# Performance work log

Hardware: AMD Instinct MI355X
Metric: run time of the kernel (lower is better)

Reference implementation:

```python
import jax, jax.numpy as jnp
import numpy as np
import math

B = 1048576
BG_RES = 512
NUM_LEVELS = 2
POWER = 4
MIPNOISE = 0.5
INIT_VAL = -2.0


def cube_face_uv(v):
    # v: [N,3] direction vectors. OpenGL cubemap face convention
    # (faces: 0:+x 1:-x 2:+y 3:-y 4:+z 5:-z), as used by nvdiffrast 'cube'.
    x, y, z = v[:, 0], v[:, 1], v[:, 2]
    ax, ay, az = jnp.abs(x), jnp.abs(y), jnp.abs(z)
    is_x = (ax >= ay) & (ax >= az)
    is_y = (~is_x) & (ay >= az)
    face = jnp.where(is_x, jnp.where(x >= 0, 0, 1),
                     jnp.where(is_y, jnp.where(y >= 0, 2, 3),
                               jnp.where(z >= 0, 4, 5))).astype(jnp.int32)
    ma = jnp.where(is_x, ax, jnp.where(is_y, ay, az))
    sc = jnp.where(is_x, jnp.where(x >= 0, -z, z),
                   jnp.where(is_y, x, jnp.where(z >= 0, x, -x)))
    tc = jnp.where(is_x, -y, jnp.where(is_y, jnp.where(y >= 0, z, -z), -y))
    u = 0.5 * (sc / ma + 1.0)
    t = 0.5 * (tc / ma + 1.0)
    return face, u, t


def build_pyramid(tex):
    # tex: [6,R,R,3] -> list of 2x2 box-filtered mips down to 1x1 (nvdiffrast style)
    levels = [tex]
    t = tex
    while t.shape[1] > 1:
        R = t.shape[1]
        t = t.reshape(6, R // 2, 2, R // 2, 2, 3).mean(axis=(2, 4))
        levels.append(t)
    return levels


def bilinear(tex, face, u, v):
    # tex: [6,R,R,3]; face/u/v: [N]. Clamp-to-edge bilinear per selected face.
    R = tex.shape[1]
    x = u * R - 0.5
    y = v * R - 0.5
    x0f = jnp.floor(x); y0f = jnp.floor(y)
    fx = (x - x0f)[:, None]; fy = (y - y0f)[:, None]
    x0 = jnp.clip(x0f.astype(jnp.int32), 0, R - 1)
    y0 = jnp.clip(y0f.astype(jnp.int32), 0, R - 1)
    x1 = jnp.clip(x0f.astype(jnp.int32) + 1, 0, R - 1)
    y1 = jnp.clip(y0f.astype(jnp.int32) + 1, 0, R - 1)
    flat = tex.reshape(6 * R * R, 3)
    base = face * (R * R)
    g00 = flat[base + y0 * R + x0]
    g01 = flat[base + y0 * R + x1]
    g10 = flat[base + y1 * R + x0]
    g11 = flat[base + y1 * R + x1]
    return ((1 - fx) * (1 - fy) * g00 + fx * (1 - fy) * g01 +
            (1 - fx) * fy * g10 + fx * fy * g11)


def sample_cubemap(tex6, face, u, v, mip):
    # trilinear: bilinear in two adjacent mips, lerp by fractional mip level
    levels = build_pyramid(tex6)
    lmax = float(len(levels) - 1)
    m = jnp.clip(mip, 0.0, lmax)
    out = jnp.zeros((face.shape[0], 3), tex6.dtype)
    for l, t in enumerate(levels):
        wl = jnp.clip(1.0 - jnp.abs(m - l), 0.0, 1.0)  # (1-f)/f trilinear weights
        out = out + wl[:, None] * bilinear(t, face, u, v)
    return out


def setup_inputs() -> dict:
    key = jax.random.key(0)
    k1, k2, k3, k4, k5 = jax.random.split(key, 5)
    viewdirs = jax.random.normal(k1, (B, 3), dtype=jnp.float32)
    viewdirs = viewdirs / jnp.linalg.norm(viewdirs, axis=-1, keepdims=True)
    saSample = jax.random.normal(k2, (B,), dtype=jnp.float32)
    noise_u = jax.random.uniform(k3, (B,), dtype=jnp.float32)
    # parameters (init_val*ones/(num_levels-i) in torch; perturbed for nontrivial grads)
    bg_mat0 = (INIT_VAL * jnp.ones((1, 6, 128, 128, 3), jnp.float32)
               + 0.1 * jax.random.normal(k4, (1, 6, 128, 128, 3), jnp.float32))
    bg_mat1 = (INIT_VAL / 2.0 * jnp.ones((1, 6, 512, 512, 3), jnp.float32)
               + 0.1 * jax.random.normal(k5, (1, 6, 512, 512, 3), jnp.float32))
    return {
        "viewdirs": viewdirs,
        "saSample": saSample,
        "noise_u": noise_u,
        "bg_mat0": bg_mat0,
        "bg_mat1": bg_mat1,
        "brightness": jnp.asarray(0.0, jnp.float32),
        "mul": jnp.asarray(1.0, jnp.float32),
        "mipbias": jnp.asarray(0.5, jnp.float32),
    }


def reference(viewdirs, saSample, noise_u, bg_mat0, bg_mat1, brightness, mul, mipbias):
    h = w = BG_RES  # from bg_mats[-1]
    # sa2mip
    distortion = 1.0 / jnp.max(jnp.abs(viewdirs), axis=-1)  # 1/||u||_inf
    saTexel = distortion / h / w
    miplevel = ((saSample - jnp.log(saTexel)) / math.log(POWER) / 2.0
                + mipbias + MIPNOISE * noise_u)
    miplevel = jnp.maximum(miplevel, 0.0)

    face, u, t = cube_face_uv(viewdirs)
    sumemb = sample_cubemap(bg_mat0[0], face, u, t, miplevel)  # mip 1 (128)
    sumemb = sumemb + sample_cubemap(bg_mat1[0], face, u, t, miplevel)  # mip 0 (512)

    # activation == 'identity' branch: exp(x).clip(0.01, 1000)
    img = jnp.clip(jnp.exp(jnp.clip(brightness, -1.0, 2.0) + mul * sumemb), 0.01, 1000.0)
    return img
```

## Files before the change

### kernel.cpp

```cpp
#include <hip/hip_runtime.h>
#include <hip/hip_bf16.h>
#include <math.h>


#define NPYR1_4 524286

__device__ __constant__ int OFFS0[7] = {0, 24576, 30720, 32256, 32640, 32736, 32760};
__device__ __constant__ int OFFS1[9] = {0, 393216, 491520, 516096, 522240,
                                        523776, 524160, 524256, 524280};
static const int H_OFFS0[7] = {0, 24576, 30720, 32256, 32640, 32736, 32760};
static const int H_OFFS1[9] = {0, 393216, 491520, 516096, 522240,
                               523776, 524160, 524256, 524280};

__device__ __constant__ int LOFF[5] = {0, 1536, 1920, 2016, 2040};

struct PyrArgs {
    const void* src;
    float4* dst[5];
    int R;
    int tpf;
    int T;
    int nlev;
};

__global__ __launch_bounds__(256) void pyr_kernel(PyrArgs a0, PyrArgs a1, int split) {
    __shared__ float4 A[32 * 32];
    __shared__ float4 Bb[16 * 16];

    PyrArgs a = (blockIdx.x < (unsigned)split) ? a0 : a1;
    int bid = (blockIdx.x < (unsigned)split) ? blockIdx.x : blockIdx.x - split;

    const int tpf = a.tpf;
    const int face = bid / (tpf * tpf);
    const int tif = bid - face * tpf * tpf;
    const int ty = tif / tpf, tx = tif - (tif / tpf) * tpf;
    const int T = a.T, R = a.R;
    const int tid = threadIdx.x;
    const int baseY = ty * T, baseX = tx * T;

    const int total = T * T;
    const float* src = (const float*)a.src;
    for (int idx = tid; idx < total; idx += 256) {
        int r = idx / T, c = idx - (idx / T) * T;
        const float* p = src + ((size_t)(face * R + baseY + r) * R + baseX + c) * 3;
        A[r * T + c] = make_float4(p[0], p[1], p[2], 0.f);
    }
    __syncthreads();

    float4* cur = A;
    float4* nxt = Bb;
    int curT = T;
    for (int l = 0; l < a.nlev; ++l) {
        const int nT = curT >> 1;
        const int Rg = R >> (l + 1);
        const int tb = T >> (l + 1);
        float4* dst = a.dst[l];
        const int n = nT * nT;
        for (int idx = tid; idx < n; idx += 256) {
            int ly = idx / nT, lx = idx - (idx / nT) * nT;
            float4 q00 = cur[(2 * ly) * curT + 2 * lx];
            float4 q01 = cur[(2 * ly) * curT + 2 * lx + 1];
            float4 q10 = cur[(2 * ly + 1) * curT + 2 * lx];
            float4 q11 = cur[(2 * ly + 1) * curT + 2 * lx + 1];
            float4 s = make_float4(0.25f * (q00.x + q01.x + q10.x + q11.x),
                                   0.25f * (q00.y + q01.y + q10.y + q11.y),
                                   0.25f * (q00.z + q01.z + q10.z + q11.z), 0.f);
            nxt[ly * nT + lx] = s;
            dst[(size_t)(face * Rg + ty * tb + ly) * Rg + tx * tb + lx] = s;
        }
        __syncthreads();
        float4* tmp = cur; cur = nxt; nxt = tmp;
        curT = nT;
    }
}


__device__ __forceinline__ void wuv(int R, float u, float v, int& x0, int& x1,
                                    int& y0, int& y1, float& fx, float& fy) {
    float xf = u * (float)R - 0.5f;
    float yf = v * (float)R - 0.5f;
    float x0f = floorf(xf), y0f = floorf(yf);
    fx = xf - x0f;
    fy = yf - y0f;
    int xi = (int)x0f, yi = (int)y0f;
    x0 = min(max(xi, 0), R - 1);
    x1 = min(max(xi + 1, 0), R - 1);
    y0 = min(max(yi, 0), R - 1);
    y1 = min(max(yi + 1, 0), R - 1);
}

__device__ __forceinline__ void bilin4(const float4* __restrict__ tex, int R,
                                       int face, float u, float v, float o[3]) {
    int x0, x1, y0, y1; float fx, fy;
    wuv(R, u, v, x0, x1, y0, y1, fx, fy);
    const float4* base = tex + (size_t)face * R * R;
    float4 p00 = base[y0 * R + x0];
    float4 p01 = base[y0 * R + x1];
    float4 p10 = base[y1 * R + x0];
    float4 p11 = base[y1 * R + x1];
    float w00 = (1.f - fx) * (1.f - fy), w01 = fx * (1.f - fy);
    float w10 = (1.f - fx) * fy, w11 = fx * fy;
    o[0] = w00 * p00.x + w01 * p01.x + w10 * p10.x + w11 * p11.x;
    o[1] = w00 * p00.y + w01 * p01.y + w10 * p10.y + w11 * p11.y;
    o[2] = w00 * p00.z + w01 * p01.z + w10 * p10.z + w11 * p11.z;
}

__device__ __forceinline__ void bilin3(const float* __restrict__ tex, int R,
                                       int face, float u, float v, float o[3]) {
    int x0, x1, y0, y1; float fx, fy;
    wuv(R, u, v, x0, x1, y0, y1, fx, fy);
    const float* base = tex + (size_t)face * R * R * 3;
    const float* p00 = base + (y0 * R + x0) * 3;
    const float* p01 = base + (y0 * R + x1) * 3;
    const float* p10 = base + (y1 * R + x0) * 3;
    const float* p11 = base + (y1 * R + x1) * 3;
    float w00 = (1.f - fx) * (1.f - fy), w01 = fx * (1.f - fy);
    float w10 = (1.f - fx) * fy, w11 = fx * fy;
#pragma unroll
    for (int c = 0; c < 3; ++c)
        o[c] = w00 * p00[c] + w01 * p01[c] + w10 * p10[c] + w11 * p11[c];
}

__device__ __forceinline__ void bilinL(const float4* __restrict__ L, int lb, int R,
                                       int face, float u, float v, float o[3]) {
    int x0, x1, y0, y1; float fx, fy;
    wuv(R, u, v, x0, x1, y0, y1, fx, fy);
    const float4* base = L + lb + face * R * R;
    float4 p00 = base[y0 * R + x0];
    float4 p01 = base[y0 * R + x1];
    float4 p10 = base[y1 * R + x0];
    float4 p11 = base[y1 * R + x1];
    float w00 = (1.f - fx) * (1.f - fy), w01 = fx * (1.f - fy);
    float w10 = (1.f - fx) * fy, w11 = fx * fy;
    o[0] = w00 * p00.x + w01 * p01.x + w10 * p10.x + w11 * p11.x;
    o[1] = w00 * p00.y + w01 * p01.y + w10 * p10.y + w11 * p11.y;
    o[2] = w00 * p00.z + w01 * p01.z + w10 * p10.z + w11 * p11.z;
}

__device__ __forceinline__ void tap1(const float4* __restrict__ L,
                                     const float* __restrict__ tex1,
                                     const float4* __restrict__ pyr1, int l,
                                     int face, float u, float v, float o[3]) {
    if (l >= 5)      bilinL(L, LOFF[l - 5], 16 >> (l - 5), face, u, v, o);
    else if (l >= 1) bilin4(pyr1 + OFFS1[l - 1], 512 >> l, face, u, v, o);
    else             bilin3(tex1, 512, face, u, v, o);
}

__device__ __forceinline__ void tap0(const float4* __restrict__ L,
                                     const float* __restrict__ tex0,
                                     const float4* __restrict__ pyr0, int l,
                                     int face, float u, float v, float o[3]) {
    if (l >= 3)      bilinL(L, 2046 + LOFF[l - 3], 16 >> (l - 3), face, u, v, o);
    else if (l >= 1) bilin4(pyr0 + OFFS0[l - 1], 128 >> l, face, u, v, o);
    else             bilin3(tex0, 128, face, u, v, o);
}

__device__ __forceinline__ void lds_reduce(float4* L, int sb, int sr, int db,
                                           int tid) {
    int dr = sr >> 1;
    int n = 6 * dr * dr;
    for (int idx = tid; idx < n; idx += 256) {
        int f = idx / (dr * dr);
        int rem = idx - f * dr * dr;
        int y = rem / dr, x = rem - y * dr;
        const float4* s = L + sb + f * sr * sr;
        float4 q00 = s[(2 * y) * sr + 2 * x];
        float4 q01 = s[(2 * y) * sr + 2 * x + 1];
        float4 q10 = s[(2 * y + 1) * sr + 2 * x];
        float4 q11 = s[(2 * y + 1) * sr + 2 * x + 1];
        L[db + f * dr * dr + y * dr + x] =
            make_float4(0.25f * (q00.x + q01.x + q10.x + q11.x),
                        0.25f * (q00.y + q01.y + q10.y + q11.y),
                        0.25f * (q00.z + q01.z + q10.z + q11.z), 0.f);
    }
}

__global__ __launch_bounds__(256) void sample_kernel(
    const float* __restrict__ vd, const float* __restrict__ sa,
    const float* __restrict__ nu, const float* __restrict__ tex0,
    const float* __restrict__ tex1, const float* __restrict__ sb,
    const float* __restrict__ sm, const float* __restrict__ smb,
    const float4* __restrict__ pyr0, const float4* __restrict__ pyr1,
    float* __restrict__ out, int n) {
    __shared__ float4 L[4092];
    const int tid = threadIdx.x;

    for (int i = tid; i < 1536; i += 256) L[i] = pyr1[OFFS1[4] + i];
    for (int i = tid; i < 1536; i += 256) L[2046 + i] = pyr0[OFFS0[2] + i];
    for (int i = tid; i < 384; i += 256)  L[3582 + i] = pyr0[OFFS0[3] + i];
    for (int i = tid; i < 96; i += 256)   L[3966 + i] = pyr0[OFFS0[4] + i];
    __syncthreads();
    lds_reduce(L, 0, 16, 1536, tid);
    lds_reduce(L, 3966, 4, 4062, tid);
    __syncthreads();
    lds_reduce(L, 1536, 8, 1920, tid);
    lds_reduce(L, 4062, 2, 4086, tid);
    __syncthreads();
    lds_reduce(L, 1920, 4, 2016, tid);
    __syncthreads();
    lds_reduce(L, 2016, 2, 2040, tid);
    __syncthreads();

    const float brightness = fminf(fmaxf(sb[0], -1.f), 2.f);
    const float mul = sm[0];
    const float mipbias = smb[0];

    const int stride = gridDim.x * 256;
    for (int i = blockIdx.x * 256 + tid; i < n; i += stride) {
        float x = vd[3 * i + 0];
        float y = vd[3 * i + 1];
        float z = vd[3 * i + 2];
        float ax = fabsf(x), ay = fabsf(y), az = fabsf(z);

        bool is_x = (ax >= ay) && (ax >= az);
        bool is_y = (!is_x) && (ay >= az);

        int face;
        float ma, sc, tc;
        if (is_x) {
            face = (x >= 0.f) ? 0 : 1;
            ma = ax; sc = (x >= 0.f) ? -z : z; tc = -y;
        } else if (is_y) {
            face = (y >= 0.f) ? 2 : 3;
            ma = ay; sc = x; tc = (y >= 0.f) ? z : -z;
        } else {
            face = (z >= 0.f) ? 4 : 5;
            ma = az; sc = (z >= 0.f) ? x : -x; tc = -y;
        }
        float u = 0.5f * (sc / ma + 1.f);
        float t = 0.5f * (tc / ma + 1.f);

        float saTexel = (1.f / ma) / 512.f / 512.f;
        float mip = (sa[i] - logf(saTexel)) / 1.3862943611198906f / 2.0f +
                    mipbias + 0.5f * nu[i];
        mip = fmaxf(mip, 0.f);

        float s0[3];
        {
            float m = fminf(mip, 7.f);
            float l0f = floorf(m);
            int l0 = (int)l0f;
            float f = m - l0f;
            tap0(L, tex0, pyr0, l0, face, u, t, s0);
            if (f > 0.f && l0 < 7) {
                float c1[3];
                tap0(L, tex0, pyr0, l0 + 1, face, u, t, c1);
                float w0 = 1.f - f;
#pragma unroll
                for (int c = 0; c < 3; ++c) s0[c] = w0 * s0[c] + f * c1[c];
            }
        }
        float s1[3];
        {
            float m = fminf(mip, 9.f);
            float l0f = floorf(m);
            int l0 = (int)l0f;
            float f = m - l0f;
            tap1(L, tex1, pyr1, l0, face, u, t, s1);
            if (f > 0.f && l0 < 9) {
                float c1[3];
                tap1(L, tex1, pyr1, l0 + 1, face, u, t, c1);
                float w0 = 1.f - f;
#pragma unroll
                for (int c = 0; c < 3; ++c) s1[c] = w0 * s1[c] + f * c1[c];
            }
        }

#pragma unroll
        for (int c = 0; c < 3; ++c) {
            float e = expf(brightness + mul * (s0[c] + s1[c]));
            out[3 * i + c] = fminf(fmaxf(e, 0.01f), 1000.f);
        }
    }
}

extern "C" void kernel_launch(void* const* d_in, const int* in_sizes, int n_in,
                              void* d_out, int out_size, void* d_ws, size_t ws_size,
                              hipStream_t stream) {
    const float* vd = (const float*)d_in[0];
    const float* sa = (const float*)d_in[1];
    const float* nu = (const float*)d_in[2];
    const float* tex0 = (const float*)d_in[3];
    const float* tex1 = (const float*)d_in[4];
    const float* br = (const float*)d_in[5];
    const float* mu = (const float*)d_in[6];
    const float* mb = (const float*)d_in[7];
    float* out = (float*)d_out;

    float4* pyr1 = (float4*)d_ws;
    float4* pyr0 = pyr1 + NPYR1_4;

    const int B = in_sizes[1];

    PyrArgs a0{}, a1{};
    a0.src = tex1; a0.R = 512; a0.tpf = 16; a0.T = 32; a0.nlev = 5;
    for (int l = 0; l < 5; ++l) a0.dst[l] = pyr1 + H_OFFS1[l];
    a1.src = tex0; a1.R = 128; a1.tpf = 4; a1.T = 32; a1.nlev = 5;
    for (int l = 0; l < 5; ++l) a1.dst[l] = pyr0 + H_OFFS0[l];
    int split1 = 6 * 16 * 16;
    int grid1 = split1 + 6 * 4 * 4;
    hipLaunchKernelGGL(pyr_kernel, dim3(grid1), dim3(256), 0, stream, a0, a1, split1);

    hipLaunchKernelGGL(sample_kernel, dim3(512), dim3(256), 0, stream,
                       vd, sa, nu, tex0, tex1, br, mu, mb, pyr0, pyr1, out, B);
}
```

Measured before the change: 143.3 us.

## Store mip pyramid in fp16, vectorize texture staging, enlarge sample grid

Mip pyramid levels in workspace and the LDS-resident small levels are now stored as packed 4x fp16 (8 bytes) instead of float4, halving gather bandwidth and LDS footprint. Pyramid tile loading reads base texels with float4 vector loads. Level offsets become closed-form expressions instead of constant-memory tables, and the sample kernel grid grows from 512 to 1280 blocks. The cost is fp16 rounding of filtered texels, including compounded rounding in the LDS reductions, which may affect accuracy.

```diff
diff --git a/kernel.cpp b/kernel.cpp
--- a/kernel.cpp
+++ b/kernel.cpp
@@ -1,22 +1,23 @@
 #include <hip/hip_runtime.h>
 #include <hip/hip_bf16.h>
+#include <hip/hip_fp16.h>
 #include <math.h>
 
 
-#define NPYR1_4 524286
-
-__device__ __constant__ int OFFS0[7] = {0, 24576, 30720, 32256, 32640, 32736, 32760};
-__device__ __constant__ int OFFS1[9] = {0, 393216, 491520, 516096, 522240,
-                                        523776, 524160, 524256, 524280};
-static const int H_OFFS0[7] = {0, 24576, 30720, 32256, 32640, 32736, 32760};
-static const int H_OFFS1[9] = {0, 393216, 491520, 516096, 522240,
-                               523776, 524160, 524256, 524280};
-
-__device__ __constant__ int LOFF[5] = {0, 1536, 1920, 2016, 2040};
+struct __align__(8) H4 { __half x, y, z, w; };
+
+#define PYR0_WS_BASE 524288
+
+__device__ __forceinline__ H4 f2h4(float a, float b, float c) {
+    H4 h;
+    h.x = __float2half(a); h.y = __float2half(b); h.z = __float2half(c);
+    h.w = __float2half(0.f);
+    return h;
+}
 
 struct PyrArgs {
-    const void* src;
-    float4* dst[5];
+    const float* src;
+    H4* dst[5];
     int R;
     int tpf;
     int T;
@@ -38,12 +39,17 @@
     const int tid = threadIdx.x;
     const int baseY = ty * T, baseX = tx * T;
 
-    const int total = T * T;
-    const float* src = (const float*)a.src;
-    for (int idx = tid; idx < total; idx += 256) {
-        int r = idx / T, c = idx - (idx / T) * T;
-        const float* p = src + ((size_t)(face * R + baseY + r) * R + baseX + c) * 3;
-        A[r * T + c] = make_float4(p[0], p[1], p[2], 0.f);
+    const int ngroups = (T * T) >> 2;
+    for (int g = tid; g < ngroups; g += 256) {
+        int r = (g * 4) / T, c = (g * 4) - ((g * 4) / T) * T;
+        const float4* p = (const float4*)(a.src +
+            ((size_t)(face * R + baseY + r) * R + baseX + c) * 3);
+        float4 q0 = p[0], q1 = p[1], q2 = p[2];
+        float4* dst = &A[r * T + c];
+        dst[0] = make_float4(q0.x, q0.y, q0.z, 0.f);
+        dst[1] = make_float4(q0.w, q1.x, q1.y, 0.f);
+        dst[2] = make_float4(q1.z, q1.w, q2.x, 0.f);
+        dst[3] = make_float4(q2.y, q2.z, q2.w, 0.f);
     }
     __syncthreads();
 
@@ -54,7 +60,7 @@
         const int nT = curT >> 1;
         const int Rg = R >> (l + 1);
         const int tb = T >> (l + 1);
-        float4* dst = a.dst[l];
+        H4* dst = a.dst[l];
         const int n = nT * nT;
         for (int idx = tid; idx < n; idx += 256) {
             int ly = idx / nT, lx = idx - (idx / nT) * nT;
@@ -62,11 +68,12 @@
             float4 q01 = cur[(2 * ly) * curT + 2 * lx + 1];
             float4 q10 = cur[(2 * ly + 1) * curT + 2 * lx];
             float4 q11 = cur[(2 * ly + 1) * curT + 2 * lx + 1];
-            float4 s = make_float4(0.25f * (q00.x + q01.x + q10.x + q11.x),
-                                   0.25f * (q00.y + q01.y + q10.y + q11.y),
-                                   0.25f * (q00.z + q01.z + q10.z + q11.z), 0.f);
-            nxt[ly * nT + lx] = s;
-            dst[(size_t)(face * Rg + ty * tb + ly) * Rg + tx * tb + lx] = s;
+            float sx = 0.25f * (q00.x + q01.x + q10.x + q11.x);
+            float sy = 0.25f * (q00.y + q01.y + q10.y + q11.y);
+            float sz = 0.25f * (q00.z + q01.z + q10.z + q11.z);
+            nxt[ly * nT + lx] = make_float4(sx, sy, sz, 0.f);
+            dst[(size_t)(face * Rg + ty * tb + ly) * Rg + tx * tb + lx] =
+                f2h4(sx, sy, sz);
         }
         __syncthreads();
         float4* tmp = cur; cur = nxt; nxt = tmp;
@@ -89,20 +96,34 @@
     y1 = min(max(yi + 1, 0), R - 1);
 }
 
-__device__ __forceinline__ void bilin4(const float4* __restrict__ tex, int R,
+__device__ __forceinline__ void mix4(H4 p00, H4 p01, H4 p10, H4 p11,
+                                     float fx, float fy, float o[3]) {
+    float w00 = (1.f - fx) * (1.f - fy), w01 = fx * (1.f - fy);
+    float w10 = (1.f - fx) * fy, w11 = fx * fy;
+    o[0] = w00 * __half2float(p00.x) + w01 * __half2float(p01.x) +
+           w10 * __half2float(p10.x) + w11 * __half2float(p11.x);
+    o[1] = w00 * __half2float(p00.y) + w01 * __half2float(p01.y) +
+           w10 * __half2float(p10.y) + w11 * __half2float(p11.y);
+    o[2] = w00 * __half2float(p00.z) + w01 * __half2float(p01.z) +
+           w10 * __half2float(p10.z) + w11 * __half2float(p11.z);
+}
+
+__device__ __forceinline__ void bilinG(const H4* __restrict__ t, int R,
                                        int face, float u, float v, float o[3]) {
     int x0, x1, y0, y1; float fx, fy;
     wuv(R, u, v, x0, x1, y0, y1, fx, fy);
-    const float4* base = tex + (size_t)face * R * R;
-    float4 p00 = base[y0 * R + x0];
-    float4 p01 = base[y0 * R + x1];
-    float4 p10 = base[y1 * R + x0];
-    float4 p11 = base[y1 * R + x1];
-    float w00 = (1.f - fx) * (1.f - fy), w01 = fx * (1.f - fy);
-    float w10 = (1.f - fx) * fy, w11 = fx * fy;
-    o[0] = w00 * p00.x + w01 * p01.x + w10 * p10.x + w11 * p11.x;
-    o[1] = w00 * p00.y + w01 * p01.y + w10 * p10.y + w11 * p11.y;
-    o[2] = w00 * p00.z + w01 * p01.z + w10 * p10.z + w11 * p11.z;
+    const H4* b = t + face * R * R;
+    mix4(b[y0 * R + x0], b[y0 * R + x1], b[y1 * R + x0], b[y1 * R + x1],
+         fx, fy, o);
+}
+
+__device__ __forceinline__ void bilinL(const H4* L, int lb, int R,
+                                       int face, float u, float v, float o[3]) {
+    int x0, x1, y0, y1; float fx, fy;
+    wuv(R, u, v, x0, x1, y0, y1, fx, fy);
+    int b = lb + face * R * R;
+    mix4(L[b + y0 * R + x0], L[b + y0 * R + x1],
+         L[b + y1 * R + x0], L[b + y1 * R + x1], fx, fy, o);
 }
 
 __device__ __forceinline__ void bilin3(const float* __restrict__ tex, int R,
@@ -121,57 +142,51 @@
         o[c] = w00 * p00[c] + w01 * p01[c] + w10 * p10[c] + w11 * p11[c];
 }
 
-__device__ __forceinline__ void bilinL(const float4* __restrict__ L, int lb, int R,
-                                       int face, float u, float v, float o[3]) {
-    int x0, x1, y0, y1; float fx, fy;
-    wuv(R, u, v, x0, x1, y0, y1, fx, fy);
-    const float4* base = L + lb + face * R * R;
-    float4 p00 = base[y0 * R + x0];
-    float4 p01 = base[y0 * R + x1];
-    float4 p10 = base[y1 * R + x0];
-    float4 p11 = base[y1 * R + x1];
-    float w00 = (1.f - fx) * (1.f - fy), w01 = fx * (1.f - fy);
-    float w10 = (1.f - fx) * fy, w11 = fx * fy;
-    o[0] = w00 * p00.x + w01 * p01.x + w10 * p10.x + w11 * p11.x;
-    o[1] = w00 * p00.y + w01 * p01.y + w10 * p10.y + w11 * p11.y;
-    o[2] = w00 * p00.z + w01 * p01.z + w10 * p10.z + w11 * p11.z;
-}
-
-__device__ __forceinline__ void tap1(const float4* __restrict__ L,
-                                     const float* __restrict__ tex1,
-                                     const float4* __restrict__ pyr1, int l,
-                                     int face, float u, float v, float o[3]) {
-    if (l >= 5)      bilinL(L, LOFF[l - 5], 16 >> (l - 5), face, u, v, o);
-    else if (l >= 1) bilin4(pyr1 + OFFS1[l - 1], 512 >> l, face, u, v, o);
-    else             bilin3(tex1, 512, face, u, v, o);
-}
-
-__device__ __forceinline__ void tap0(const float4* __restrict__ L,
-                                     const float* __restrict__ tex0,
-                                     const float4* __restrict__ pyr0, int l,
-                                     int face, float u, float v, float o[3]) {
-    if (l >= 3)      bilinL(L, 2046 + LOFF[l - 3], 16 >> (l - 3), face, u, v, o);
-    else if (l >= 1) bilin4(pyr0 + OFFS0[l - 1], 128 >> l, face, u, v, o);
-    else             bilin3(tex0, 128, face, u, v, o);
-}
-
-__device__ __forceinline__ void lds_reduce(float4* L, int sb, int sr, int db,
-                                           int tid) {
+__device__ __forceinline__ void lds_reduce(H4* L, int sb, int sr, int db, int tid) {
     int dr = sr >> 1;
     int n = 6 * dr * dr;
     for (int idx = tid; idx < n; idx += 256) {
         int f = idx / (dr * dr);
         int rem = idx - f * dr * dr;
         int y = rem / dr, x = rem - y * dr;
-        const float4* s = L + sb + f * sr * sr;
-        float4 q00 = s[(2 * y) * sr + 2 * x];
-        float4 q01 = s[(2 * y) * sr + 2 * x + 1];
-        float4 q10 = s[(2 * y + 1) * sr + 2 * x];
-        float4 q11 = s[(2 * y + 1) * sr + 2 * x + 1];
-        L[db + f * dr * dr + y * dr + x] =
-            make_float4(0.25f * (q00.x + q01.x + q10.x + q11.x),
-                        0.25f * (q00.y + q01.y + q10.y + q11.y),
-                        0.25f * (q00.z + q01.z + q10.z + q11.z), 0.f);
+        const H4* s = L + sb + f * sr * sr;
+        H4 q00 = s[(2 * y) * sr + 2 * x];
+        H4 q01 = s[(2 * y) * sr + 2 * x + 1];
+        H4 q10 = s[(2 * y + 1) * sr + 2 * x];
+        H4 q11 = s[(2 * y + 1) * sr + 2 * x + 1];
+        L[db + f * dr * dr + y * dr + x] = f2h4(
+            0.25f * (__half2float(q00.x) + __half2float(q01.x) +
+                     __half2float(q10.x) + __half2float(q11.x)),
+            0.25f * (__half2float(q00.y) + __half2float(q01.y) +
+                     __half2float(q10.y) + __half2float(q11.y)),
+            0.25f * (__half2float(q00.z) + __half2float(q01.z) +
+                     __half2float(q10.z) + __half2float(q11.z)));
+    }
+}
+
+__device__ __forceinline__ void tap1(const H4* L, const float* __restrict__ tex1,
+                                     const H4* __restrict__ g1, int l,
+                                     int face, float u, float v, float o[3]) {
+    if (l >= 5) {
+        int j = l - 5;
+        bilinL(L, 2048 - (2048 >> (2 * j)), 16 >> j, face, u, v, o);
+    } else if (l >= 1) {
+        bilinG(g1 + (524288 - (524288 >> (2 * (l - 1)))), 512 >> l, face, u, v, o);
+    } else {
+        bilin3(tex1, 512, face, u, v, o);
+    }
+}
+
+__device__ __forceinline__ void tap0(const H4* L, const float* __restrict__ tex0,
+                                     const H4* __restrict__ g0, int l,
+                                     int face, float u, float v, float o[3]) {
+    if (l >= 3) {
+        int j = l - 3;
+        bilinL(L, 2046 + 2048 - (2048 >> (2 * j)), 16 >> j, face, u, v, o);
+    } else if (l >= 1) {
+        bilinG(g0 + (32768 - (32768 >> (2 * (l - 1)))), 128 >> l, face, u, v, o);
+    } else {
+        bilin3(tex0, 128, face, u, v, o);
     }
 }
 
@@ -180,15 +195,15 @@
     const float* __restrict__ nu, const float* __restrict__ tex0,
     const float* __restrict__ tex1, const float* __restrict__ sb,
     const float* __restrict__ sm, const float* __restrict__ smb,
-    const float4* __restrict__ pyr0, const float4* __restrict__ pyr1,
+    const H4* __restrict__ g1, const H4* __restrict__ g0,
     float* __restrict__ out, int n) {
-    __shared__ float4 L[4092];
+    __shared__ H4 L[4092];
     const int tid = threadIdx.x;
 
-    for (int i = tid; i < 1536; i += 256) L[i] = pyr1[OFFS1[4] + i];
-    for (int i = tid; i < 1536; i += 256) L[2046 + i] = pyr0[OFFS0[2] + i];
-    for (int i = tid; i < 384; i += 256)  L[3582 + i] = pyr0[OFFS0[3] + i];
-    for (int i = tid; i < 96; i += 256)   L[3966 + i] = pyr0[OFFS0[4] + i];
+    for (int i = tid; i < 1536; i += 256) L[i] = g1[522240 + i];
+    for (int i = tid; i < 1536; i += 256) L[2046 + i] = g0[30720 + i];
+    for (int i = tid; i < 384; i += 256)  L[3582 + i] = g0[32256 + i];
+    for (int i = tid; i < 96; i += 256)   L[3966 + i] = g0[32640 + i];
     __syncthreads();
     lds_reduce(L, 0, 16, 1536, tid);
     lds_reduce(L, 3966, 4, 4062, tid);
@@ -241,10 +256,10 @@
             float l0f = floorf(m);
             int l0 = (int)l0f;
             float f = m - l0f;
-            tap0(L, tex0, pyr0, l0, face, u, t, s0);
+            tap0(L, tex0, g0, l0, face, u, t, s0);
             if (f > 0.f && l0 < 7) {
                 float c1[3];
-                tap0(L, tex0, pyr0, l0 + 1, face, u, t, c1);
+                tap0(L, tex0, g0, l0 + 1, face, u, t, c1);
                 float w0 = 1.f - f;
 #pragma unroll
                 for (int c = 0; c < 3; ++c) s0[c] = w0 * s0[c] + f * c1[c];
@@ -256,10 +271,10 @@
             float l0f = floorf(m);
             int l0 = (int)l0f;
             float f = m - l0f;
-            tap1(L, tex1, pyr1, l0, face, u, t, s1);
+            tap1(L, tex1, g1, l0, face, u, t, s1);
             if (f > 0.f && l0 < 9) {
                 float c1[3];
-                tap1(L, tex1, pyr1, l0 + 1, face, u, t, c1);
+                tap1(L, tex1, g1, l0 + 1, face, u, t, c1);
                 float w0 = 1.f - f;
 #pragma unroll
                 for (int c = 0; c < 3; ++c) s1[c] = w0 * s1[c] + f * c1[c];
@@ -287,20 +302,23 @@
     const float* mb = (const float*)d_in[7];
     float* out = (float*)d_out;
 
-    float4* pyr1 = (float4*)d_ws;
-    float4* pyr0 = pyr1 + NPYR1_4;
+    H4* g1 = (H4*)d_ws;
+    H4* g0 = g1 + PYR0_WS_BASE;
 
     const int B = in_sizes[1];
+
+    static const int O1[5] = {0, 393216, 491520, 516096, 522240};
+    static const int O0[5] = {0, 24576, 30720, 32256, 32640};
 
     PyrArgs a0{}, a1{};
     a0.src = tex1; a0.R = 512; a0.tpf = 16; a0.T = 32; a0.nlev = 5;
-    for (int l = 0; l < 5; ++l) a0.dst[l] = pyr1 + H_OFFS1[l];
+    for (int l = 0; l < 5; ++l) a0.dst[l] = g1 + O1[l];
     a1.src = tex0; a1.R = 128; a1.tpf = 4; a1.T = 32; a1.nlev = 5;
-    for (int l = 0; l < 5; ++l) a1.dst[l] = pyr0 + H_OFFS0[l];
+    for (int l = 0; l < 5; ++l) a1.dst[l] = g0 + O0[l];
     int split1 = 6 * 16 * 16;
     int grid1 = split1 + 6 * 4 * 4;
     hipLaunchKernelGGL(pyr_kernel, dim3(grid1), dim3(256), 0, stream, a0, a1, split1);
 
-    hipLaunchKernelGGL(sample_kernel, dim3(512), dim3(256), 0, stream,
-                       vd, sa, nu, tex0, tex1, br, mu, mb, pyr0, pyr1, out, B);
-}
+    hipLaunchKernelGGL(sample_kernel, dim3(1280), dim3(256), 0, stream,
+                       vd, sa, nu, tex0, tex1, br, mu, mb, g1, g0, out, B);
+}
```

Measured after the change: 138.6 us. 1.03x faster.
